# Optimization experiments

Measured on AMD Instinct MI355X. Metric: run time of the kernel, lower is better.

The kernel has to match this reference:

```python
import jax, jax.numpy as jnp
import numpy as np

EMBED_DIM = 1024
NUM_HEADS = 16
HEAD_DIM = EMBED_DIM // NUM_HEADS


def setup_inputs() -> dict:
    key = jax.random.key(0)
    ks = jax.random.split(key, 5)
    B, S, D = 2, 2048, EMBED_DIM
    scale = 1.0 / np.sqrt(D)
    x = jax.random.normal(ks[0], (B, S, D), dtype=jnp.float32)
    qkv_w = jax.random.uniform(ks[1], (3 * D, D), dtype=jnp.float32, minval=-scale, maxval=scale)
    qkv_b = jax.random.uniform(ks[2], (3 * D,), dtype=jnp.float32, minval=-scale, maxval=scale)
    out_w = jax.random.uniform(ks[3], (D, D), dtype=jnp.float32, minval=-scale, maxval=scale)
    out_b = jax.random.uniform(ks[4], (D,), dtype=jnp.float32, minval=-scale, maxval=scale)
    return {"x": x, "qkv_w": qkv_w, "qkv_b": qkv_b, "out_w": out_w, "out_b": out_b}


def reference(x, qkv_w, qkv_b, out_w, out_b):
    B, S, D = x.shape
    H, hd = NUM_HEADS, HEAD_DIM
    # QKV projection (torch Linear: y = x @ W^T + b)
    qkv = jnp.einsum('bsd,ed->bse', x, qkv_w) + qkv_b          # [B,S,3D]
    qkv = qkv.reshape(B, S, 3, H, hd)
    q, k, v = (jnp.moveaxis(qkv[:, :, i], 2, 1) for i in range(3))  # each [B,H,S,hd]
    scores = jnp.einsum('bhqd,bhkd->bhqk', q, k) / np.sqrt(hd)  # [B,H,S,S]
    probs = jax.nn.softmax(scores, axis=-1)
    attn = jnp.einsum('bhqk,bhkd->bhqd', probs, v)              # [B,H,S,hd]
    attn = jnp.moveaxis(attn, 1, 2).reshape(B, S, D)
    return jnp.einsum('bsd,ed->bse', attn, out_w) + out_b
```

## Files before the change

kernel.cpp:

```cpp
#include <hip/hip_runtime.h>
#include <stdint.h>

typedef __bf16 bf16;
typedef __attribute__((ext_vector_type(2))) __bf16 bf16x2;
typedef __attribute__((ext_vector_type(4))) __bf16 bf16x4;
typedef __attribute__((ext_vector_type(8))) __bf16 bf16x8;
typedef __attribute__((ext_vector_type(4))) float f32x4;
typedef __attribute__((ext_vector_type(16))) float f32x16;

#define LOG2E_OVER_8 0.18033688011112042f

#if __has_builtin(__builtin_amdgcn_exp2f)
#define EXP2(x) __builtin_amdgcn_exp2f(x)
#else
#define EXP2(x) exp2f(x)
#endif

__device__ __forceinline__ void gl_lds16(const bf16* g, bf16* l) {
  __builtin_amdgcn_global_load_lds(
      (const __attribute__((address_space(1))) void*)g,
      (__attribute__((address_space(3))) void*)l, 16, 0, 0);
}
#define WAIT_VM0_BARRIER() asm volatile("s_waitcnt vmcnt(0)\n\ts_barrier" ::: "memory")

__device__ __forceinline__ uint32_t pack2(float a, float b) {
  union { bf16x2 v; uint32_t u; } z;
  z.v[0] = (bf16)a; z.v[1] = (bf16)b;
  return z.u;
}

__device__ __forceinline__ void pl32swap(uint32_t& a, uint32_t& b) {
  asm("v_permlane32_swap_b32 %0, %1" : "+v"(a), "+v"(b));
}

#define N_X  (4096 * 1024)
#define N_WQ (3072 * 1024)
#define N_WO (1024 * 1024)
__global__ __launch_bounds__(256) void cvt3_kernel(const float* __restrict__ x,
                                                   const float* __restrict__ wq,
                                                   const float* __restrict__ wo,
                                                   bf16* __restrict__ d) {
  int i = (blockIdx.x * 256 + threadIdx.x) * 8;
  const float* s;
  if (i < N_X) s = x + i;
  else if (i < N_X + N_WQ) s = wq + (i - N_X);
  else s = wo + (i - N_X - N_WQ);
  float4 a = *(const float4*)s;
  float4 b = *(const float4*)(s + 4);
  bf16x8 o;
  o[0] = (bf16)a.x; o[1] = (bf16)a.y; o[2] = (bf16)a.z; o[3] = (bf16)a.w;
  o[4] = (bf16)b.x; o[5] = (bf16)b.y; o[6] = (bf16)b.z; o[7] = (bf16)b.w;
  *(bf16x8*)(d + i) = o;
}

template <int EPI>
__global__ __launch_bounds__(256, 3) void gemm_bt(
    const bf16* __restrict__ A, const bf16* __restrict__ Bw,
    const float* __restrict__ bias,
    bf16* __restrict__ qo, bf16* __restrict__ ko, bf16* __restrict__ vTo,
    float* __restrict__ outF) {
  constexpr int MT = EPI ? 64 : 128;
  constexpr int MI = MT / 32;
  constexpr int BK = EPI ? 64 : 32;
  constexpr int NC = BK / 32;
  constexpr int NIT = 1024 / BK;
  constexpr int ASZ = MT * BK;
  constexpr int BSZ = 128 * BK;
  constexpr int RS = 136;
  constexpr int SME0 = 2 * ASZ + 2 * BSZ;
  constexpr int SME = EPI ? SME0 : (SME0 > 128 * RS ? SME0 : 128 * RS);
  __shared__ __attribute__((aligned(16))) bf16 smem[SME];

  int bx, by;
  {
    const int f = blockIdx.x;
    const int xcd = f & 7, idx = f >> 3;
    if constexpr (EPI == 0) { by = xcd * 4 + (idx & 3); bx = idx >> 2; }
    else                    { by = xcd * 8 + (idx & 7); bx = idx >> 3; }
  }

  const int t = threadIdx.x;
  const int L = t & 63;
  const int li = L & 15;
  const int qd = L >> 4;
  const int w = t >> 6;
  const int wm = (w >> 1) * (MT / 2);
  const int wn = (w & 1) * 64;
  const int bm0 = by * MT;
  const int bn0 = bx * 128;
  const int r_st = t >> 2;
  const int c_st = (t & 3) * 8;

  const bf16* Ab = A + (size_t)bm0 * 1024;
  const bf16* Bb = Bw + (size_t)bn0 * 1024;

  auto issue = [&](int k0, int bi) {
    bf16* As_ = smem + bi * ASZ;
    bf16* Bs_ = smem + 2 * ASZ + bi * BSZ;
#pragma unroll
    for (int kc = 0; kc < NC; ++kc) {
      const int kk = k0 + kc * 32;
      gl_lds16(Ab + (size_t)r_st * 1024 + kk + c_st, As_ + kc * MT * 32 + t * 8);
      if constexpr (MT == 128)
        gl_lds16(Ab + (size_t)(r_st + 64) * 1024 + kk + c_st,
                 As_ + kc * MT * 32 + (t + 256) * 8);
      gl_lds16(Bb + (size_t)r_st * 1024 + kk + c_st, Bs_ + kc * 4096 + t * 8);
      gl_lds16(Bb + (size_t)(r_st + 64) * 1024 + kk + c_st,
               Bs_ + kc * 4096 + (t + 256) * 8);
    }
  };

  f32x4 acc[MI][4] = {};
  issue(0, 0);
  for (int it = 0; it < NIT; ++it) {
    WAIT_VM0_BARRIER();
    if (it < NIT - 1) issue((it + 1) * BK, (it + 1) & 1);
    const bf16* Ac = smem + (it & 1) * ASZ;
    const bf16* Bc = smem + 2 * ASZ + (it & 1) * BSZ;
#pragma unroll
    for (int kc = 0; kc < NC; ++kc) {
      const bf16* Ak = Ac + kc * MT * 32;
      const bf16* Bk = Bc + kc * 4096;
      bf16x8 af[MI], bfr[4];
#pragma unroll
      for (int mi = 0; mi < MI; ++mi)
        af[mi] = *(const bf16x8*)(Ak + (wm + mi * 16 + li) * 32 + qd * 8);
#pragma unroll
      for (int ni = 0; ni < 4; ++ni)
        bfr[ni] = *(const bf16x8*)(Bk + (wn + ni * 16 + li) * 32 + qd * 8);
#pragma unroll
      for (int mi = 0; mi < MI; ++mi)
#pragma unroll
        for (int ni = 0; ni < 4; ++ni)
          acc[mi][ni] = __builtin_amdgcn_mfma_f32_16x16x32_bf16(
              af[mi], bfr[ni], acc[mi][ni], 0, 0, 0);
    }
  }

  if constexpr (EPI == 0) {
    const int which = bn0 >> 10;
    __syncthreads();
    bf16* Ct = smem;
    if (which == 2) {
#pragma unroll
      for (int mi = 0; mi < MI; ++mi) {
        const int m_l = wm + mi * 16 + qd * 4;
#pragma unroll
        for (int ni = 0; ni < 4; ++ni) {
          const int n_l = wn + ni * 16 + li;
          const float bi = bias[bn0 + n_l];
          bf16x4 pk;
#pragma unroll
          for (int r = 0; r < 4; ++r) pk[r] = (bf16)(acc[mi][ni][r] + bi);
          *(bf16x4*)(Ct + n_l * RS + m_l) = pk;
        }
      }
    } else {
      const float sc = (which == 0) ? LOG2E_OVER_8 : 1.0f;
#pragma unroll
      for (int mi = 0; mi < MI; ++mi) {
        const int m_l = wm + mi * 16 + qd * 4;
#pragma unroll
        for (int ni = 0; ni < 4; ++ni) {
          const int n_l = wn + ni * 16 + li;
          const float bi = bias[bn0 + n_l];
#pragma unroll
          for (int r = 0; r < 4; ++r)
            Ct[(m_l + r) * RS + n_l] = (bf16)((acc[mi][ni][r] + bi) * sc);
        }
      }
    }
    __syncthreads();
    const int jr = t >> 4;
    const int jc = t & 15;
#pragma unroll
    for (int pass = 0; pass < 8; ++pass) {
      const int row = pass * 16 + jr;
      bf16x8 vv = *(const bf16x8*)(Ct + row * RS + jc * 8);
      if (which == 2) {
        const int n_g = bn0 + row;
        const int hh = (n_g >> 6) & 15, dd = n_g & 63;
        const int bb = bm0 >> 11;
        const int s_b = (bm0 & 2047) + jc * 8;
        *(bf16x8*)(vTo + ((size_t)(bb * 16 + hh) * 64 + dd) * 2048 + s_b) = vv;
      } else {
        const int m_g = bm0 + row;
        const int bb = m_g >> 11, ss = m_g & 2047;
        const int n_g = bn0 + jc * 8;
        const int hh = (n_g >> 6) & 15, dd = n_g & 63;
        bf16* dst = (which == 0 ? qo : ko);
        *(bf16x8*)(dst + ((size_t)(bb * 16 + hh) * 2048 + ss) * 64 + dd) = vv;
      }
    }
  } else {
#pragma unroll
    for (int mi = 0; mi < MI; ++mi) {
      const int m_g = bm0 + wm + mi * 16 + qd * 4;
#pragma unroll
      for (int ni = 0; ni < 4; ++ni) {
        const int n_g = bn0 + wn + ni * 16 + li;
        const float bi = bias[n_g];
#pragma unroll
        for (int r = 0; r < 4; ++r)
          outF[(size_t)(m_g + r) * 1024 + n_g] = acc[mi][ni][r] + bi;
      }
    }
  }
}

__global__ __launch_bounds__(256, 2) void attn_fwd(
    const bf16* __restrict__ Q, const bf16* __restrict__ K,
    const bf16* __restrict__ VT, bf16* __restrict__ AO) {
  __shared__ __attribute__((aligned(16))) bf16 Ks[2 * 8192];
  __shared__ __attribute__((aligned(16))) bf16 Vs[2 * 8192];
  const int t = threadIdx.x;
  const int L = t & 63;
  const int m31 = L & 31;
  const int hi = L >> 5;
  const int w = t >> 6;

  const int lid = blockIdx.x;
  const int bh_ = ((lid & 7) << 2) + (lid >> 7);
  const int qb = (lid >> 3) & 15;
  const int b = bh_ >> 4, h = bh_ & 15;
  const size_t bh = (size_t)(b * 16 + h);

  const bf16* Qp = Q + bh * 2048 * 64;
  const bf16* Kp = K + bh * 2048 * 64;
  const bf16* Vp = VT + bh * 64 * 2048;
  const int q0 = qb * 128 + w * 32;

  bf16x8 qf[4];
#pragma unroll
  for (int s = 0; s < 4; ++s)
    qf[s] = *(const bf16x8*)(Qp + (size_t)(q0 + m31) * 64 + s * 16 + hi * 8);

  f32x16 acc[2][2] = {};
  float ls[4] = {0.f, 0.f, 0.f, 0.f};

  const int srow = t >> 3;
  const int scc = (t & 7) ^ (srow & 7);
  auto issue = [&](int it2, int bi) {
#pragma unroll
    for (int tile = 0; tile < 2; ++tile) {
      const int kt = it2 * 2 + tile;
      const bf16* Kt = Kp + (size_t)kt * 4096;
      const bf16* Vt = Vp + kt * 64;
      bf16* Kd = Ks + bi * 8192 + tile * 4096;
      bf16* Vd = Vs + bi * 8192 + tile * 4096;
#pragma unroll
      for (int r = 0; r < 2; ++r) {
        gl_lds16(Kt + (srow + 32 * r) * 64 + scc * 8, Kd + (t + 256 * r) * 8);
        gl_lds16(Vt + (size_t)(srow + 32 * r) * 2048 + scc * 8, Vd + (t + 256 * r) * 8);
      }
    }
  };

  const int rlow = m31 & 7;
  union FU { uint32_t u[4]; bf16x8 v; };

  issue(0, 0);
  for (int it2 = 0; it2 < 16; ++it2) {
    WAIT_VM0_BARRIER();
    if (it2 < 15) issue(it2 + 1, (it2 + 1) & 1);
    const bf16* Kc0 = Ks + (it2 & 1) * 8192;
    const bf16* Vc0 = Vs + (it2 & 1) * 8192;

    auto QKT = [&](int tile, int kt2) -> f32x16 {
      const bf16* Kc = Kc0 + tile * 4096;
      f32x16 z = {};
      __builtin_amdgcn_s_setprio(1);
#pragma unroll
      for (int s = 0; s < 4; ++s) {
        bf16x8 kf = *(const bf16x8*)(
            Kc + ((kt2 * 32 + m31) * 8 + ((2 * s + hi) ^ rlow)) * 8);
        z = __builtin_amdgcn_mfma_f32_32x32x16_bf16(kf, qf[s], z, 0, 0, 0);
      }
      __builtin_amdgcn_s_setprio(0);
      return z;
    };

    auto SM = [&](const f32x16& st, int gi, FU* afp) {
      uint32_t pk[8];
      float lsl = 0.f;
#pragma unroll
      for (int j = 0; j < 8; ++j) {
        float a = EXP2(st[2 * j]);
        float c = EXP2(st[2 * j + 1]);
        lsl += a + c;
        pk[j] = pack2(a, c);
      }
      ls[gi] += lsl;
      pl32swap(pk[0], pk[2]);
      pl32swap(pk[1], pk[3]);
      pl32swap(pk[4], pk[6]);
      pl32swap(pk[5], pk[7]);
      afp[0].u[0] = pk[0]; afp[0].u[1] = pk[1];
      afp[0].u[2] = pk[2]; afp[0].u[3] = pk[3];
      afp[1].u[0] = pk[4]; afp[1].u[1] = pk[5];
      afp[1].u[2] = pk[6]; afp[1].u[3] = pk[7];
    };

    auto PV = [&](int tile, int kt2, const FU* afp) {
      const bf16* Vc = Vc0 + tile * 4096;
      __builtin_amdgcn_s_setprio(1);
#pragma unroll
      for (int dt = 0; dt < 2; ++dt)
#pragma unroll
        for (int u = 0; u < 2; ++u) {
          bf16x8 vf = *(const bf16x8*)(
              Vc + ((dt * 32 + m31) * 8 + ((kt2 * 4 + u * 2 + hi) ^ rlow)) * 8);
          acc[dt][tile] = __builtin_amdgcn_mfma_f32_32x32x16_bf16(
              afp[u].v, vf, acc[dt][tile], 0, 0, 0);
        }
      __builtin_amdgcn_s_setprio(0);
    };

    FU A0[2], A1[2], A2[2], A3[2];
    f32x16 st0 = QKT(0, 0);
    f32x16 st1 = QKT(0, 1);
    SM(st0, 0, A0);
    f32x16 st2 = QKT(1, 0);
    PV(0, 0, A0);
    SM(st1, 1, A1);
    f32x16 st3 = QKT(1, 1);
    PV(0, 1, A1);
    SM(st2, 2, A2);
    PV(1, 0, A2);
    SM(st3, 3, A3);
    PV(1, 1, A3);
  }

  f32x16 accf[2];
#pragma unroll
  for (int dt = 0; dt < 2; ++dt) accf[dt] = acc[dt][0] + acc[dt][1];
  float lsum = (ls[0] + ls[1]) + (ls[2] + ls[3]);
  lsum += __shfl_xor(lsum, 32);
  const float inv = 1.f / lsum;

#pragma unroll
  for (int r = 0; r < 16; ++r) {
    const int qrow = (r & 3) + 8 * (r >> 2) + 4 * hi;
    const float invq = __shfl(inv, qrow);
    const size_t base = ((size_t)b * 2048 + q0 + qrow) * 1024 + h * 64 + m31;
    AO[base] = (bf16)(accf[0][r] * invq);
    AO[base + 32] = (bf16)(accf[1][r] * invq);
  }
}

extern "C" void kernel_launch(void* const* d_in, const int* in_sizes, int n_in,
                              void* d_out, int out_size, void* d_ws, size_t ws_size,
                              hipStream_t stream) {
  const float* x = (const float*)d_in[0];
  const float* qkvw = (const float*)d_in[1];
  const float* qkvb = (const float*)d_in[2];
  const float* outw = (const float*)d_in[3];
  const float* outb = (const float*)d_in[4];
  float* out = (float*)d_out;

  bf16* xb = (bf16*)d_ws;
  bf16* wq = xb + (size_t)N_X;
  bf16* wo = wq + (size_t)N_WQ;
  bf16* q = wo + (size_t)N_WO;
  bf16* kk = q + (size_t)2 * 16 * 2048 * 64;
  bf16* vT = kk + (size_t)2 * 16 * 2048 * 64;
  bf16* attn = xb;

  cvt3_kernel<<<4096, 256, 0, stream>>>(x, qkvw, outw, xb);

  gemm_bt<0><<<768, 256, 0, stream>>>(xb, wq, qkvb, q, kk, vT, nullptr);
  attn_fwd<<<512, 256, 0, stream>>>(q, kk, vT, attn);
  gemm_bt<1><<<512, 256, 0, stream>>>(attn, wo, outb, nullptr, nullptr, nullptr, out);
}
```

Measured before the change: 175.7 us.

## Process 64 query rows per wave in attention to reuse K/V fragments

Each wave in the attention kernel now handles two 32-row query sub-tiles (256 queries per block), so every K and V fragment read from LDS feeds two MFMAs, halving LDS traffic per FLOP and halving the grid to 256 blocks. The inner loop is rewritten as a software pipeline that computes QK^T for the next key tile while softmax and PV run on the current one. The cost is more registers per thread (launch bounds drop to 1 block/SM) and only 256 blocks on 256 CUs, so there is less occupancy and latency hiding.

```diff
diff --git a/kernel.cpp b/kernel.cpp
--- a/kernel.cpp
+++ b/kernel.cpp
@@ -208,7 +208,7 @@
   }
 }
 
-__global__ __launch_bounds__(256, 2) void attn_fwd(
+__global__ __launch_bounds__(256, 1) void attn_fwd(
     const bf16* __restrict__ Q, const bf16* __restrict__ K,
     const bf16* __restrict__ VT, bf16* __restrict__ AO) {
   __shared__ __attribute__((aligned(16))) bf16 Ks[2 * 8192];
@@ -220,23 +220,26 @@
   const int w = t >> 6;
 
   const int lid = blockIdx.x;
-  const int bh_ = ((lid & 7) << 2) + (lid >> 7);
-  const int qb = (lid >> 3) & 15;
+  const int bh_ = ((lid & 7) << 2) + (lid >> 6);
+  const int qb = (lid >> 3) & 7;
   const int b = bh_ >> 4, h = bh_ & 15;
   const size_t bh = (size_t)(b * 16 + h);
 
   const bf16* Qp = Q + bh * 2048 * 64;
   const bf16* Kp = K + bh * 2048 * 64;
   const bf16* Vp = VT + bh * 64 * 2048;
-  const int q0 = qb * 128 + w * 32;
-
-  bf16x8 qf[4];
-#pragma unroll
-  for (int s = 0; s < 4; ++s)
-    qf[s] = *(const bf16x8*)(Qp + (size_t)(q0 + m31) * 64 + s * 16 + hi * 8);
+  const int q0 = qb * 256 + w * 64;
+
+  bf16x8 qf[2][4];
+#pragma unroll
+  for (int qs = 0; qs < 2; ++qs)
+#pragma unroll
+    for (int s = 0; s < 4; ++s)
+      qf[qs][s] = *(const bf16x8*)(
+          Qp + (size_t)(q0 + qs * 32 + m31) * 64 + s * 16 + hi * 8);
 
   f32x16 acc[2][2] = {};
-  float ls[4] = {0.f, 0.f, 0.f, 0.f};
+  float ls[2][2] = {};
 
   const int srow = t >> 3;
   const int scc = (t & 7) ^ (srow & 7);
@@ -266,21 +269,26 @@
     const bf16* Kc0 = Ks + (it2 & 1) * 8192;
     const bf16* Vc0 = Vs + (it2 & 1) * 8192;
 
-    auto QKT = [&](int tile, int kt2) -> f32x16 {
-      const bf16* Kc = Kc0 + tile * 4096;
-      f32x16 z = {};
+    auto QKT = [&](int kt, f32x16* st2) {
+      const bf16* Kc = Kc0 + (kt >> 1) * 4096;
+      bf16x8 kf[4];
+#pragma unroll
+      for (int s = 0; s < 4; ++s)
+        kf[s] = *(const bf16x8*)(
+            Kc + (((kt & 1) * 32 + m31) * 8 + ((2 * s + hi) ^ rlow)) * 8);
       __builtin_amdgcn_s_setprio(1);
 #pragma unroll
-      for (int s = 0; s < 4; ++s) {
-        bf16x8 kf = *(const bf16x8*)(
-            Kc + ((kt2 * 32 + m31) * 8 + ((2 * s + hi) ^ rlow)) * 8);
-        z = __builtin_amdgcn_mfma_f32_32x32x16_bf16(kf, qf[s], z, 0, 0, 0);
+      for (int qs = 0; qs < 2; ++qs) {
+        f32x16 z = {};
+#pragma unroll
+        for (int s = 0; s < 4; ++s)
+          z = __builtin_amdgcn_mfma_f32_32x32x16_bf16(kf[s], qf[qs][s], z, 0, 0, 0);
+        st2[qs] = z;
       }
       __builtin_amdgcn_s_setprio(0);
-      return z;
     };
 
-    auto SM = [&](const f32x16& st, int gi, FU* afp) {
+    auto SM = [&](const f32x16& st, int qs, int kt, FU* afp) {
       uint32_t pk[8];
       float lsl = 0.f;
 #pragma unroll
@@ -290,7 +298,7 @@
         lsl += a + c;
         pk[j] = pack2(a, c);
       }
-      ls[gi] += lsl;
+      ls[qs][kt & 1] += lsl;
       pl32swap(pk[0], pk[2]);
       pl32swap(pk[1], pk[3]);
       pl32swap(pk[4], pk[6]);
@@ -301,51 +309,56 @@
       afp[1].u[2] = pk[6]; afp[1].u[3] = pk[7];
     };
 
-    auto PV = [&](int tile, int kt2, const FU* afp) {
-      const bf16* Vc = Vc0 + tile * 4096;
+    auto PV = [&](int kt, FU A[2][2]) {
+      const bf16* Vc = Vc0 + (kt >> 1) * 4096;
       __builtin_amdgcn_s_setprio(1);
 #pragma unroll
       for (int dt = 0; dt < 2; ++dt)
 #pragma unroll
         for (int u = 0; u < 2; ++u) {
           bf16x8 vf = *(const bf16x8*)(
-              Vc + ((dt * 32 + m31) * 8 + ((kt2 * 4 + u * 2 + hi) ^ rlow)) * 8);
-          acc[dt][tile] = __builtin_amdgcn_mfma_f32_32x32x16_bf16(
-              afp[u].v, vf, acc[dt][tile], 0, 0, 0);
+              Vc + ((dt * 32 + m31) * 8 + (((kt & 1) * 4 + u * 2 + hi) ^ rlow)) * 8);
+#pragma unroll
+          for (int qs = 0; qs < 2; ++qs)
+            acc[dt][qs] = __builtin_amdgcn_mfma_f32_32x32x16_bf16(
+                A[qs][u].v, vf, acc[dt][qs], 0, 0, 0);
         }
       __builtin_amdgcn_s_setprio(0);
     };
 
-    FU A0[2], A1[2], A2[2], A3[2];
-    f32x16 st0 = QKT(0, 0);
-    f32x16 st1 = QKT(0, 1);
-    SM(st0, 0, A0);
-    f32x16 st2 = QKT(1, 0);
-    PV(0, 0, A0);
-    SM(st1, 1, A1);
-    f32x16 st3 = QKT(1, 1);
-    PV(0, 1, A1);
-    SM(st2, 2, A2);
-    PV(1, 0, A2);
-    SM(st3, 3, A3);
-    PV(1, 1, A3);
-  }
-
-  f32x16 accf[2];
-#pragma unroll
-  for (int dt = 0; dt < 2; ++dt) accf[dt] = acc[dt][0] + acc[dt][1];
-  float lsum = (ls[0] + ls[1]) + (ls[2] + ls[3]);
-  lsum += __shfl_xor(lsum, 32);
-  const float inv = 1.f / lsum;
-
-#pragma unroll
-  for (int r = 0; r < 16; ++r) {
-    const int qrow = (r & 3) + 8 * (r >> 2) + 4 * hi;
-    const float invq = __shfl(inv, qrow);
-    const size_t base = ((size_t)b * 2048 + q0 + qrow) * 1024 + h * 64 + m31;
-    AO[base] = (bf16)(accf[0][r] * invq);
-    AO[base + 32] = (bf16)(accf[1][r] * invq);
-  }
+    f32x16 stc[2], stn[2];
+    QKT(0, stc);
+#pragma unroll
+    for (int kt = 0; kt < 4; ++kt) {
+      if (kt < 3) QKT(kt + 1, stn);
+      FU A[2][2];
+      SM(stc[0], 0, kt, A[0]);
+      SM(stc[1], 1, kt, A[1]);
+      PV(kt, A);
+      stc[0] = stn[0];
+      stc[1] = stn[1];
+    }
+  }
+
+  float inv[2];
+#pragma unroll
+  for (int qs = 0; qs < 2; ++qs) {
+    float l = ls[qs][0] + ls[qs][1];
+    l += __shfl_xor(l, 32);
+    inv[qs] = 1.f / l;
+  }
+
+#pragma unroll
+  for (int qs = 0; qs < 2; ++qs)
+#pragma unroll
+    for (int r = 0; r < 16; ++r) {
+      const int qrow = (r & 3) + 8 * (r >> 2) + 4 * hi;
+      const float invq = __shfl(inv[qs], qrow);
+      const size_t base =
+          ((size_t)b * 2048 + q0 + qs * 32 + qrow) * 1024 + h * 64 + m31;
+      AO[base] = (bf16)(acc[0][qs][r] * invq);
+      AO[base + 32] = (bf16)(acc[1][qs][r] * invq);
+    }
 }
 
 extern "C" void kernel_launch(void* const* d_in, const int* in_sizes, int n_in,
@@ -369,6 +382,6 @@
   cvt3_kernel<<<4096, 256, 0, stream>>>(x, qkvw, outw, xb);
 
   gemm_bt<0><<<768, 256, 0, stream>>>(xb, wq, qkvb, q, kk, vT, nullptr);
-  attn_fwd<<<512, 256, 0, stream>>>(q, kk, vT, attn);
+  attn_fwd<<<256, 256, 0, stream>>>(q, kk, vT, attn);
   gemm_bt<1><<<512, 256, 0, stream>>>(attn, wo, outb, nullptr, nullptr, nullptr, out);
 }
```

Result: slower. 182.9 us (+4.1%).

## Split attention KV range across two thread halves with LDS reduction

Applied to the files above, without the earlier changes.

Doubles the attention block to 512 threads. Each 256-thread half processes half of the key/value sequence for the same 128 queries, using its own double-buffered LDS region. The two partial accumulators and row sums are then combined through shared memory before normalising and writing. This doubles the wave count per block to hide latency better. In exchange it adds an LDS exchange and extra barriers, and it drops the previous interleaved QK/softmax/PV schedule in favour of a simpler sequential loop.

```diff
diff --git a/kernel.cpp b/kernel.cpp
--- a/kernel.cpp
+++ b/kernel.cpp
@@ -208,16 +208,17 @@
   }
 }
 
-__global__ __launch_bounds__(256, 2) void attn_fwd(
+__global__ __launch_bounds__(512, 2) void attn_fwd(
     const bf16* __restrict__ Q, const bf16* __restrict__ K,
     const bf16* __restrict__ VT, bf16* __restrict__ AO) {
-  __shared__ __attribute__((aligned(16))) bf16 Ks[2 * 8192];
-  __shared__ __attribute__((aligned(16))) bf16 Vs[2 * 8192];
+  __shared__ __attribute__((aligned(16))) bf16 smem[32768];
   const int t = threadIdx.x;
+  const int half = t >> 8;
+  const int tt = t & 255;
   const int L = t & 63;
   const int m31 = L & 31;
-  const int hi = L >> 5;
-  const int w = t >> 6;
+  const int hi = (L >> 5) & 1;
+  const int w4 = (t >> 6) & 3;
 
   const int lid = blockIdx.x;
   const int bh_ = ((lid & 7) << 2) + (lid >> 7);
@@ -226,125 +227,127 @@
   const size_t bh = (size_t)(b * 16 + h);
 
   const bf16* Qp = Q + bh * 2048 * 64;
-  const bf16* Kp = K + bh * 2048 * 64;
-  const bf16* Vp = VT + bh * 64 * 2048;
-  const int q0 = qb * 128 + w * 32;
+  const bf16* Kp = K + bh * 2048 * 64 + (size_t)half * 1024 * 64;
+  const bf16* Vp = VT + bh * 64 * 2048 + half * 1024;
+  const int q0 = qb * 128 + w4 * 32;
 
   bf16x8 qf[4];
 #pragma unroll
   for (int s = 0; s < 4; ++s)
     qf[s] = *(const bf16x8*)(Qp + (size_t)(q0 + m31) * 64 + s * 16 + hi * 8);
 
-  f32x16 acc[2][2] = {};
-  float ls[4] = {0.f, 0.f, 0.f, 0.f};
-
-  const int srow = t >> 3;
-  const int scc = (t & 7) ^ (srow & 7);
-  auto issue = [&](int it2, int bi) {
-#pragma unroll
-    for (int tile = 0; tile < 2; ++tile) {
-      const int kt = it2 * 2 + tile;
-      const bf16* Kt = Kp + (size_t)kt * 4096;
-      const bf16* Vt = Vp + kt * 64;
-      bf16* Kd = Ks + bi * 8192 + tile * 4096;
-      bf16* Vd = Vs + bi * 8192 + tile * 4096;
-#pragma unroll
-      for (int r = 0; r < 2; ++r) {
-        gl_lds16(Kt + (srow + 32 * r) * 64 + scc * 8, Kd + (t + 256 * r) * 8);
-        gl_lds16(Vt + (size_t)(srow + 32 * r) * 2048 + scc * 8, Vd + (t + 256 * r) * 8);
-      }
+  f32x16 acc[2] = {};
+  float ls[2] = {0.f, 0.f};
+
+  bf16* Kbase = smem + half * 16384;
+  bf16* Vbase = Kbase + 8192;
+
+  const int srow = tt >> 3;
+  const int scc = (tt & 7) ^ (srow & 7);
+  auto issue = [&](int itK, int bi) {
+    const bf16* Kt = Kp + (size_t)itK * 4096;
+    const bf16* Vt = Vp + itK * 64;
+    bf16* Kd = Kbase + bi * 4096;
+    bf16* Vd = Vbase + bi * 4096;
+#pragma unroll
+    for (int r = 0; r < 2; ++r) {
+      gl_lds16(Kt + (srow + 32 * r) * 64 + scc * 8, Kd + (tt + 256 * r) * 8);
+      gl_lds16(Vt + (size_t)(srow + 32 * r) * 2048 + scc * 8, Vd + (tt + 256 * r) * 8);
     }
   };
 
   const int rlow = m31 & 7;
   union FU { uint32_t u[4]; bf16x8 v; };
 
+  auto SM = [&](const f32x16& st, int kt, FU* afp) {
+    uint32_t pk[8];
+    float lsl = 0.f;
+#pragma unroll
+    for (int j = 0; j < 8; ++j) {
+      float a = EXP2(st[2 * j]);
+      float c = EXP2(st[2 * j + 1]);
+      lsl += a + c;
+      pk[j] = pack2(a, c);
+    }
+    ls[kt] += lsl;
+    pl32swap(pk[0], pk[2]);
+    pl32swap(pk[1], pk[3]);
+    pl32swap(pk[4], pk[6]);
+    pl32swap(pk[5], pk[7]);
+    afp[0].u[0] = pk[0]; afp[0].u[1] = pk[1];
+    afp[0].u[2] = pk[2]; afp[0].u[3] = pk[3];
+    afp[1].u[0] = pk[4]; afp[1].u[1] = pk[5];
+    afp[1].u[2] = pk[6]; afp[1].u[3] = pk[7];
+  };
+
   issue(0, 0);
-  for (int it2 = 0; it2 < 16; ++it2) {
+  for (int itK = 0; itK < 16; ++itK) {
     WAIT_VM0_BARRIER();
-    if (it2 < 15) issue(it2 + 1, (it2 + 1) & 1);
-    const bf16* Kc0 = Ks + (it2 & 1) * 8192;
-    const bf16* Vc0 = Vs + (it2 & 1) * 8192;
-
-    auto QKT = [&](int tile, int kt2) -> f32x16 {
-      const bf16* Kc = Kc0 + tile * 4096;
+    if (itK < 15) issue(itK + 1, (itK + 1) & 1);
+    const bf16* Kc = Kbase + (itK & 1) * 4096;
+    const bf16* Vc = Vbase + (itK & 1) * 4096;
+
+#pragma unroll
+    for (int kt = 0; kt < 2; ++kt) {
       f32x16 z = {};
       __builtin_amdgcn_s_setprio(1);
 #pragma unroll
       for (int s = 0; s < 4; ++s) {
         bf16x8 kf = *(const bf16x8*)(
-            Kc + ((kt2 * 32 + m31) * 8 + ((2 * s + hi) ^ rlow)) * 8);
+            Kc + ((kt * 32 + m31) * 8 + ((2 * s + hi) ^ rlow)) * 8);
         z = __builtin_amdgcn_mfma_f32_32x32x16_bf16(kf, qf[s], z, 0, 0, 0);
       }
       __builtin_amdgcn_s_setprio(0);
-      return z;
-    };
-
-    auto SM = [&](const f32x16& st, int gi, FU* afp) {
-      uint32_t pk[8];
-      float lsl = 0.f;
-#pragma unroll
-      for (int j = 0; j < 8; ++j) {
-        float a = EXP2(st[2 * j]);
-        float c = EXP2(st[2 * j + 1]);
-        lsl += a + c;
-        pk[j] = pack2(a, c);
-      }
-      ls[gi] += lsl;
-      pl32swap(pk[0], pk[2]);
-      pl32swap(pk[1], pk[3]);
-      pl32swap(pk[4], pk[6]);
-      pl32swap(pk[5], pk[7]);
-      afp[0].u[0] = pk[0]; afp[0].u[1] = pk[1];
-      afp[0].u[2] = pk[2]; afp[0].u[3] = pk[3];
-      afp[1].u[0] = pk[4]; afp[1].u[1] = pk[5];
-      afp[1].u[2] = pk[6]; afp[1].u[3] = pk[7];
-    };
-
-    auto PV = [&](int tile, int kt2, const FU* afp) {
-      const bf16* Vc = Vc0 + tile * 4096;
+
+      FU A[2];
+      SM(z, kt, A);
+
       __builtin_amdgcn_s_setprio(1);
 #pragma unroll
       for (int dt = 0; dt < 2; ++dt)
 #pragma unroll
         for (int u = 0; u < 2; ++u) {
           bf16x8 vf = *(const bf16x8*)(
-              Vc + ((dt * 32 + m31) * 8 + ((kt2 * 4 + u * 2 + hi) ^ rlow)) * 8);
-          acc[dt][tile] = __builtin_amdgcn_mfma_f32_32x32x16_bf16(
-              afp[u].v, vf, acc[dt][tile], 0, 0, 0);
+              Vc + ((dt * 32 + m31) * 8 + ((kt * 4 + u * 2 + hi) ^ rlow)) * 8);
+          acc[dt] = __builtin_amdgcn_mfma_f32_32x32x16_bf16(A[u].v, vf, acc[dt],
+                                                            0, 0, 0);
         }
       __builtin_amdgcn_s_setprio(0);
-    };
-
-    FU A0[2], A1[2], A2[2], A3[2];
-    f32x16 st0 = QKT(0, 0);
-    f32x16 st1 = QKT(0, 1);
-    SM(st0, 0, A0);
-    f32x16 st2 = QKT(1, 0);
-    PV(0, 0, A0);
-    SM(st1, 1, A1);
-    f32x16 st3 = QKT(1, 1);
-    PV(0, 1, A1);
-    SM(st2, 2, A2);
-    PV(1, 0, A2);
-    SM(st3, 3, A3);
-    PV(1, 1, A3);
-  }
-
-  f32x16 accf[2];
-#pragma unroll
-  for (int dt = 0; dt < 2; ++dt) accf[dt] = acc[dt][0] + acc[dt][1];
-  float lsum = (ls[0] + ls[1]) + (ls[2] + ls[3]);
-  lsum += __shfl_xor(lsum, 32);
-  const float inv = 1.f / lsum;
-
-#pragma unroll
-  for (int r = 0; r < 16; ++r) {
-    const int qrow = (r & 3) + 8 * (r >> 2) + 4 * hi;
-    const float invq = __shfl(inv, qrow);
-    const size_t base = ((size_t)b * 2048 + q0 + qrow) * 1024 + h * 64 + m31;
-    AO[base] = (bf16)(accf[0][r] * invq);
-    AO[base + 32] = (bf16)(accf[1][r] * invq);
+    }
+  }
+
+  float lsum = ls[0] + ls[1];
+  __syncthreads();
+  float* xch = (float*)smem;
+  float* rec = xch + (size_t)(w4 * 64 + L) * 33;
+  if (half == 1) {
+#pragma unroll
+    for (int dt = 0; dt < 2; ++dt)
+#pragma unroll
+      for (int r = 0; r < 16; ++r)
+        rec[dt * 16 + r] = acc[dt][r];
+    rec[32] = lsum;
+  }
+  __syncthreads();
+  if (half == 0) {
+#pragma unroll
+    for (int dt = 0; dt < 2; ++dt)
+#pragma unroll
+      for (int r = 0; r < 16; ++r)
+        acc[dt][r] += rec[dt * 16 + r];
+    lsum += rec[32];
+
+    lsum += __shfl_xor(lsum, 32);
+    const float inv = 1.f / lsum;
+
+#pragma unroll
+    for (int r = 0; r < 16; ++r) {
+      const int qrow = (r & 3) + 8 * (r >> 2) + 4 * hi;
+      const float invq = __shfl(inv, qrow);
+      const size_t base = ((size_t)b * 2048 + q0 + qrow) * 1024 + h * 64 + m31;
+      AO[base] = (bf16)(acc[0][r] * invq);
+      AO[base + 32] = (bf16)(acc[1][r] * invq);
+    }
   }
 }
 
@@ -369,6 +372,6 @@
   cvt3_kernel<<<4096, 256, 0, stream>>>(x, qkvw, outw, xb);
 
   gemm_bt<0><<<768, 256, 0, stream>>>(xb, wq, qkvb, q, kk, vT, nullptr);
-  attn_fwd<<<512, 256, 0, stream>>>(q, kk, vT, attn);
+  attn_fwd<<<512, 512, 0, stream>>>(q, kk, vT, attn);
   gemm_bt<1><<<512, 256, 0, stream>>>(attn, wo, outb, nullptr, nullptr, nullptr, out);
 }
```

New measurement: 171.9 us. 1.02x faster.
